# Optimization experiments

Measured on AMD Instinct MI355X. Metric: run time of the kernel, lower is better.

The kernel has to match this reference:

```python
import jax, jax.numpy as jnp
import numpy as np

L, D = 6, 2048


def setup_inputs() -> dict:
    key = jax.random.key(0)
    ks = jax.random.split(key, 6)
    # 0.05 scale keeps repeated matrix compositions numerically tame
    W_upper = jax.random.normal(ks[0], (L, D, D), dtype=jnp.float32) * 0.05
    W_lower = jax.random.normal(ks[1], (L, D, D), dtype=jnp.float32) * 0.05
    b_upper = jax.random.normal(ks[2], (L, D), dtype=jnp.float32)
    b_lower = jax.random.normal(ks[3], (L, D), dtype=jnp.float32)
    ub = jax.random.normal(ks[4], (L, D), dtype=jnp.float32)
    lb = jax.random.normal(ks[5], (L, D), dtype=jnp.float32)
    return dict(W_upper=W_upper, W_lower=W_lower, b_upper=b_upper,
                b_lower=b_lower, ub=ub, lb=lb)


def _pos(W):
    # M * W  where M = (W >= 0)
    return jnp.where(W >= 0, W, jnp.zeros_like(W))


def _neg(W):
    # ~M * W where M = (W >= 0)
    return jnp.where(W >= 0, jnp.zeros_like(W), W)


def reference(W_upper, W_lower, b_upper, b_lower, ub, lb):
    # Layer index L-1 is `self`; backsubstitute toward layer 0 (input layer).
    Wu, Wl = W_upper[-1], W_lower[-1]          # [D, D]
    bu, bl = b_upper[-1], b_lower[-1]          # [D]
    best_ub, best_lb = ub[-1], lb[-1]          # [D]
    n_layers = W_upper.shape[0]
    for i in range(n_layers - 2, -1, -1):      # prev = layer i
        Wu_p, Wu_n = _pos(Wu), _neg(Wu)
        Wl_p, Wl_n = _pos(Wl), _neg(Wl)
        # concrete bounds through prev's pre-activation bounds
        cur_ub = Wu_p @ ub[i] + Wu_n @ lb[i] + bu
        cur_lb = Wl_p @ lb[i] + Wl_n @ ub[i] + bl
        best_ub = jnp.minimum(best_ub, cur_ub)
        best_lb = jnp.maximum(best_lb, cur_lb)
        # compose symbolic bounds with prev layer's relaxation
        bu = Wu_p @ b_upper[i] + Wu_n @ b_lower[i] + bu
        bl = Wl_p @ b_lower[i] + Wl_n @ b_upper[i] + bl
        Wu = Wu_p @ W_upper[i] + Wu_n @ W_lower[i]
        Wl = Wl_p @ W_lower[i] + Wl_n @ W_upper[i]
    # final concretization against the input layer's bounds (layer 0)
    Wu_p, Wu_n = _pos(Wu), _neg(Wu)
    Wl_p, Wl_n = _pos(Wl), _neg(Wl)
    cur_ub = Wu_p @ ub[0] + Wu_n @ lb[0] + bu
    cur_lb = Wl_p @ lb[0] + Wl_n @ ub[0] + bl
    best_ub = jnp.minimum(best_ub, cur_ub)
    best_lb = jnp.maximum(best_lb, cur_lb)
    return best_ub, best_lb
```

## Files before the change

kernel.cpp:

```cpp
#include <hip/hip_runtime.h>

#define D 2048
#define DD ((size_t)D * (size_t)D)

typedef __attribute__((ext_vector_type(8))) short bf16x8;
typedef __attribute__((ext_vector_type(16))) float f32x16;

#define GLOBAL_AS __attribute__((address_space(1)))
#define LDS_AS __attribute__((address_space(3)))

__device__ inline unsigned short f2bf(float f) {
  unsigned u = __float_as_uint(f);
  u += 0x7fffu + ((u >> 16) & 1u);
  return (unsigned short)(u >> 16);
}

__global__ void init_vecs(const float* __restrict__ b_upper5,
                          const float* __restrict__ b_lower5,
                          const float* __restrict__ ub5,
                          const float* __restrict__ lb5,
                          float* __restrict__ bu, float* __restrict__ bl,
                          float* __restrict__ out) {
  int t = blockIdx.x * blockDim.x + threadIdx.x;
  if (t < D) {
    bu[t] = b_upper5[t];
    bl[t] = b_lower5[t];
    out[t] = ub5[t];
    out[D + t] = lb5[t];
  }
}

__global__ __launch_bounds__(256) void prep(
    const float* __restrict__ Wu, const float* __restrict__ Wl,
    const float* __restrict__ ubi, const float* __restrict__ lbi,
    const float* __restrict__ bupi, const float* __restrict__ bloi,
    float* __restrict__ bu, float* __restrict__ bl,
    float* __restrict__ best,
    unsigned short* __restrict__ oU, unsigned short* __restrict__ oL,
    const float* __restrict__ Wup, const float* __restrict__ Wlo,
    unsigned short* __restrict__ BsT, unsigned short* __restrict__ BdT,
    int update_bias, int write16) {
  __shared__ float red[4][4];
  __shared__ unsigned short sS[64][68];
  __shared__ unsigned short sD[64][68];

  const int t = threadIdx.x;

  if (blockIdx.x < 2048) {
    const int r = blockIdx.x;
    const size_t base = (size_t)r * D + t * 8;
    const int c = t * 8;

    float4 wu0 = *(const float4*)(Wu + base), wu1 = *(const float4*)(Wu + base + 4);
    float4 wl0 = *(const float4*)(Wl + base), wl1 = *(const float4*)(Wl + base + 4);
    float4 u0 = *(const float4*)(ubi + c),  u1 = *(const float4*)(ubi + c + 4);
    float4 l0 = *(const float4*)(lbi + c),  l1 = *(const float4*)(lbi + c + 4);
    float4 p0 = *(const float4*)(bupi + c), p1 = *(const float4*)(bupi + c + 4);
    float4 n0 = *(const float4*)(bloi + c), n1 = *(const float4*)(bloi + c + 4);

    float wu[8] = {wu0.x, wu0.y, wu0.z, wu0.w, wu1.x, wu1.y, wu1.z, wu1.w};
    float wl[8] = {wl0.x, wl0.y, wl0.z, wl0.w, wl1.x, wl1.y, wl1.z, wl1.w};
    float uu[8] = {u0.x, u0.y, u0.z, u0.w, u1.x, u1.y, u1.z, u1.w};
    float ll[8] = {l0.x, l0.y, l0.z, l0.w, l1.x, l1.y, l1.z, l1.w};
    float pp[8] = {p0.x, p0.y, p0.z, p0.w, p1.x, p1.y, p1.z, p1.w};
    float nn[8] = {n0.x, n0.y, n0.z, n0.w, n1.x, n1.y, n1.z, n1.w};

    float su_c = 0.f, su_b = 0.f, sl_c = 0.f, sl_b = 0.f;
    #pragma unroll
    for (int j = 0; j < 8; ++j) {
      su_c += wu[j] * (wu[j] >= 0.f ? uu[j] : ll[j]);
      su_b += wu[j] * (wu[j] >= 0.f ? pp[j] : nn[j]);
      sl_c += wl[j] * (wl[j] >= 0.f ? ll[j] : uu[j]);
      sl_b += wl[j] * (wl[j] >= 0.f ? nn[j] : pp[j]);
    }

    if (write16) {
      uint4 w;
      w.x = f2bf(wu[0]) | ((unsigned)f2bf(wu[1]) << 16);
      w.y = f2bf(wu[2]) | ((unsigned)f2bf(wu[3]) << 16);
      w.z = f2bf(wu[4]) | ((unsigned)f2bf(wu[5]) << 16);
      w.w = f2bf(wu[6]) | ((unsigned)f2bf(wu[7]) << 16);
      *(uint4*)(oU + base) = w;
      w.x = f2bf(wl[0]) | ((unsigned)f2bf(wl[1]) << 16);
      w.y = f2bf(wl[2]) | ((unsigned)f2bf(wl[3]) << 16);
      w.z = f2bf(wl[4]) | ((unsigned)f2bf(wl[5]) << 16);
      w.w = f2bf(wl[6]) | ((unsigned)f2bf(wl[7]) << 16);
      *(uint4*)(oL + base) = w;
    }

    #pragma unroll
    for (int off = 32; off; off >>= 1) {
      su_c += __shfl_down(su_c, off);
      su_b += __shfl_down(su_b, off);
      sl_c += __shfl_down(sl_c, off);
      sl_b += __shfl_down(sl_b, off);
    }
    int wave = t >> 6;
    if ((t & 63) == 0) {
      red[0][wave] = su_c; red[1][wave] = su_b;
      red[2][wave] = sl_c; red[3][wave] = sl_b;
    }
    __syncthreads();
    if (t == 0) {
      float a = red[0][0] + red[0][1] + red[0][2] + red[0][3];
      float b = red[1][0] + red[1][1] + red[1][2] + red[1][3];
      float cc = red[2][0] + red[2][1] + red[2][2] + red[2][3];
      float d = red[3][0] + red[3][1] + red[3][2] + red[3][3];
      float bu_old = bu[r], bl_old = bl[r];
      best[r]     = fminf(best[r],     a + bu_old);
      best[D + r] = fmaxf(best[D + r], cc + bl_old);
      if (update_bias) {
        bu[r] = b + bu_old;
        bl[r] = d + bl_old;
      }
    }
  } else {
    const int bx = blockIdx.x - 2048;
    const int k0 = (bx >> 5) * 64, c0 = (bx & 31) * 64;
    const int tx = t & 15, ty = t >> 4;
    #pragma unroll
    for (int r = 0; r < 4; ++r) {
      int kk = ty + r * 16;
      size_t g = (size_t)(k0 + kk) * D + c0 + tx * 4;
      float4 up = *(const float4*)(Wup + g);
      float4 lo = *(const float4*)(Wlo + g);
      sS[kk][tx * 4 + 0] = f2bf((up.x + lo.x) * 0.5f);
      sS[kk][tx * 4 + 1] = f2bf((up.y + lo.y) * 0.5f);
      sS[kk][tx * 4 + 2] = f2bf((up.z + lo.z) * 0.5f);
      sS[kk][tx * 4 + 3] = f2bf((up.w + lo.w) * 0.5f);
      sD[kk][tx * 4 + 0] = f2bf((up.x - lo.x) * 0.5f);
      sD[kk][tx * 4 + 1] = f2bf((up.y - lo.y) * 0.5f);
      sD[kk][tx * 4 + 2] = f2bf((up.z - lo.z) * 0.5f);
      sD[kk][tx * 4 + 3] = f2bf((up.w - lo.w) * 0.5f);
    }
    __syncthreads();
    #pragma unroll
    for (int r = 0; r < 4; ++r) {
      int cc = ty + r * 16;
      int kq = tx * 4;
      unsigned a0 = sS[kq + 0][cc] | ((unsigned)sS[kq + 1][cc] << 16);
      unsigned a1 = sS[kq + 2][cc] | ((unsigned)sS[kq + 3][cc] << 16);
      *(uint2*)(BsT + (size_t)(c0 + cc) * D + k0 + kq) = make_uint2(a0, a1);
      a0 = sD[kq + 0][cc] | ((unsigned)sD[kq + 1][cc] << 16);
      a1 = sD[kq + 2][cc] | ((unsigned)sD[kq + 3][cc] << 16);
      *(uint2*)(BdT + (size_t)(c0 + cc) * D + k0 + kq) = make_uint2(a0, a1);
    }
  }
}

__global__ __launch_bounds__(512, 2) void gemm_fused(
    const unsigned short* __restrict__ w16U,
    const unsigned short* __restrict__ w16L,
    const unsigned short* __restrict__ BsT,
    const unsigned short* __restrict__ BdT,
    float* __restrict__ Cu, float* __restrict__ Cl) {
  extern __shared__ unsigned char lds[];

  const int bid = blockIdx.x;
  const int vid = (bid & 7) * 32 + (bid >> 3);
  const int row0 = (vid >> 4) * 128, col0 = (vid & 15) * 128;

  const int tid = threadIdx.x;
  const int lane = tid & 63, wid = tid >> 6;
  const int grp = wid >> 2;
  const int w2 = wid & 3;
  const int wr = w2 >> 1, wc = w2 & 1;
  const int l31 = lane & 31, kh = lane >> 5;

  const int srow8 = lane >> 3;
  const int slot  = lane & 7;
  int rowc[2], swel[2];
  #pragma unroll
  for (int c = 0; c < 2; ++c) {
    rowc[c] = (wid + c * 8) * 8 + srow8;
    swel[c] = (slot ^ (rowc[c] & 7)) * 8;
  }
  const unsigned short* gAU[2]; const unsigned short* gAL[2];
  const unsigned short* gBs[2]; const unsigned short* gBd[2];
  #pragma unroll
  for (int c = 0; c < 2; ++c) {
    gAU[c] = w16U + (size_t)(row0 + rowc[c]) * D + swel[c];
    gAL[c] = w16L + (size_t)(row0 + rowc[c]) * D + swel[c];
    gBs[c] = BsT + (size_t)(col0 + rowc[c]) * D + swel[c];
    gBd[c] = BdT + (size_t)(col0 + rowc[c]) * D + swel[c];
  }

  f32x16 acc[2][2] = {};

  int aoff[2][4], boff[2][4];
  #pragma unroll
  for (int mb = 0; mb < 2; ++mb) {
    int ar = wr * 64 + mb * 32 + l31;
    #pragma unroll
    for (int ks = 0; ks < 4; ++ks)
      aoff[mb][ks] = ar * 128 + (((ks * 2 + kh) ^ (ar & 7)) * 16);
  }
  #pragma unroll
  for (int nb = 0; nb < 2; ++nb) {
    int bc = wc * 64 + nb * 32 + l31;
    #pragma unroll
    for (int ks = 0; ks < 4; ++ks)
      boff[nb][ks] = bc * 128 + (((ks * 2 + kh) ^ (bc & 7)) * 16);
  }

  #define STAGE(curb, kt)                                                          \
    do {                                                                           \
      unsigned bb = (unsigned)(curb) * 65536u;                                     \
      _Pragma("unroll")                                                            \
      for (int c = 0; c < 2; ++c) {                                                \
        unsigned dst = bb + (unsigned)(wid + c * 8) * 1024u;                       \
        __builtin_amdgcn_global_load_lds((const GLOBAL_AS unsigned*)(gAU[c] + (kt)),\
            (LDS_AS unsigned*)(lds + 0 + dst), 16, 0, 0);                          \
        __builtin_amdgcn_global_load_lds((const GLOBAL_AS unsigned*)(gAL[c] + (kt)),\
            (LDS_AS unsigned*)(lds + 16384 + dst), 16, 0, 0);                      \
        __builtin_amdgcn_global_load_lds((const GLOBAL_AS unsigned*)(gBs[c] + (kt)),\
            (LDS_AS unsigned*)(lds + 32768 + dst), 16, 0, 0);                      \
        __builtin_amdgcn_global_load_lds((const GLOBAL_AS unsigned*)(gBd[c] + (kt)),\
            (LDS_AS unsigned*)(lds + 49152 + dst), 16, 0, 0);                      \
      }                                                                            \
    } while (0)

  STAGE(0, 0);
  __syncthreads();

  int cur = 0;
  const unsigned Abase = grp ? 16384u : 0u;
  for (int t = 0; t < 32; ++t) {
    if (t < 31) STAGE(cur ^ 1, (t + 1) * 64);

    const unsigned char* Ab = lds + Abase + cur * 65536;
    const unsigned char* Sb = lds + 32768 + cur * 65536;
    const unsigned char* Db = lds + 49152 + cur * 65536;

    #pragma unroll
    for (int ks = 0; ks < 4; ++ks) {
      bf16x8 aw0 = *(const bf16x8*)(Ab + aoff[0][ks]);
      bf16x8 aw1 = *(const bf16x8*)(Ab + aoff[1][ks]);
      bf16x8 bs0 = *(const bf16x8*)(Sb + boff[0][ks]);
      bf16x8 bs1 = *(const bf16x8*)(Sb + boff[1][ks]);
      bf16x8 bd0 = *(const bf16x8*)(Db + boff[0][ks]);
      bf16x8 bd1 = *(const bf16x8*)(Db + boff[1][ks]);
      if (grp) { bd0 ^= (short)0x8000; bd1 ^= (short)0x8000; }
      bf16x8 av0 = aw0 & (short)0x7fff;
      bf16x8 av1 = aw1 & (short)0x7fff;

      acc[0][0] = __builtin_amdgcn_mfma_f32_32x32x16_bf16(aw0, bs0, acc[0][0], 0, 0, 0);
      acc[0][0] = __builtin_amdgcn_mfma_f32_32x32x16_bf16(av0, bd0, acc[0][0], 0, 0, 0);
      acc[0][1] = __builtin_amdgcn_mfma_f32_32x32x16_bf16(aw0, bs1, acc[0][1], 0, 0, 0);
      acc[0][1] = __builtin_amdgcn_mfma_f32_32x32x16_bf16(av0, bd1, acc[0][1], 0, 0, 0);
      acc[1][0] = __builtin_amdgcn_mfma_f32_32x32x16_bf16(aw1, bs0, acc[1][0], 0, 0, 0);
      acc[1][0] = __builtin_amdgcn_mfma_f32_32x32x16_bf16(av1, bd0, acc[1][0], 0, 0, 0);
      acc[1][1] = __builtin_amdgcn_mfma_f32_32x32x16_bf16(aw1, bs1, acc[1][1], 0, 0, 0);
      acc[1][1] = __builtin_amdgcn_mfma_f32_32x32x16_bf16(av1, bd1, acc[1][1], 0, 0, 0);
    }

    __syncthreads();
    cur ^= 1;
  }
  #undef STAGE

  float* C = grp ? Cl : Cu;
  #pragma unroll
  for (int mb = 0; mb < 2; ++mb)
    #pragma unroll
    for (int nb = 0; nb < 2; ++nb) {
      const int colg = col0 + wc * 64 + nb * 32 + l31;
      const int rowb = row0 + wr * 64 + mb * 32 + kh * 4;
      #pragma unroll
      for (int g = 0; g < 4; ++g)
        #pragma unroll
        for (int j = 0; j < 4; ++j)
          C[(size_t)(rowb + g * 8 + j) * D + colg] = acc[mb][nb][g * 4 + j];
    }
}

extern "C" void kernel_launch(void* const* d_in, const int* in_sizes, int n_in,
                              void* d_out, int out_size, void* d_ws, size_t ws_size,
                              hipStream_t stream) {
  const float* W_upper = (const float*)d_in[0];
  const float* W_lower = (const float*)d_in[1];
  const float* b_upper = (const float*)d_in[2];
  const float* b_lower = (const float*)d_in[3];
  const float* ub      = (const float*)d_in[4];
  const float* lb      = (const float*)d_in[5];
  float* out = (float*)d_out;
  float* ws  = (float*)d_ws;

  float* curU = ws;
  float* curL = ws + DD;
  unsigned short* w16U = (unsigned short*)(ws + 2 * DD);
  unsigned short* w16L = w16U + DD;
  unsigned short* BsT  = w16L + DD;
  unsigned short* BdT  = BsT + DD;
  float* bu = (float*)(BdT + DD);
  float* bl = bu + D;

  static_cast<void>(hipFuncSetAttribute(
      (const void*)gemm_fused, hipFuncAttributeMaxDynamicSharedMemorySize, 131072));

  init_vecs<<<(D + 255) / 256, 256, 0, stream>>>(
      b_upper + 5 * D, b_lower + 5 * D, ub + 5 * D, lb + 5 * D, bu, bl, out);

  const float* cU = W_upper + 5 * DD;
  const float* cL = W_lower + 5 * DD;
  for (int i = 4; i >= 0; --i) {
    prep<<<3072, 256, 0, stream>>>(cU, cL, ub + (size_t)i * D, lb + (size_t)i * D,
                                   b_upper + (size_t)i * D, b_lower + (size_t)i * D,
                                   bu, bl, out, w16U, w16L,
                                   W_upper + (size_t)i * DD, W_lower + (size_t)i * DD,
                                   BsT, BdT, 1, 1);
    gemm_fused<<<256, 512, 131072, stream>>>(w16U, w16L, BsT, BdT, curU, curL);
    cU = curU; cL = curL;
  }
  prep<<<2048, 256, 0, stream>>>(cU, cL, ub, lb, b_upper, b_lower,
                                 bu, bl, out, w16U, w16L,
                                 (const float*)nullptr, (const float*)nullptr,
                                 (unsigned short*)nullptr, (unsigned short*)nullptr,
                                 0, 0);
}
```

Measured before the change: 460.1 us.

## Use four-stage LDS pipeline with smaller K tiles and interleaved async loads

Result: slower. 510.6 us (+11.0%).

```diff
diff --git a/kernel.cpp b/kernel.cpp
--- a/kernel.cpp
+++ b/kernel.cpp
@@ -167,83 +167,83 @@
   const int wr = w2 >> 1, wc = w2 & 1;
   const int l31 = lane & 31, kh = lane >> 5;
 
-  const int srow8 = lane >> 3;
-  const int slot  = lane & 7;
-  int rowc[2], swel[2];
-  #pragma unroll
-  for (int c = 0; c < 2; ++c) {
-    rowc[c] = (wid + c * 8) * 8 + srow8;
-    swel[c] = (slot ^ (rowc[c] & 7)) * 8;
-  }
-  const unsigned short* gAU[2]; const unsigned short* gAL[2];
-  const unsigned short* gBs[2]; const unsigned short* gBd[2];
-  #pragma unroll
-  for (int c = 0; c < 2; ++c) {
-    gAU[c] = w16U + (size_t)(row0 + rowc[c]) * D + swel[c];
-    gAL[c] = w16L + (size_t)(row0 + rowc[c]) * D + swel[c];
-    gBs[c] = BsT + (size_t)(col0 + rowc[c]) * D + swel[c];
-    gBd[c] = BdT + (size_t)(col0 + rowc[c]) * D + swel[c];
-  }
+  const int rowc = wid * 16 + (lane >> 2);
+  const int swel = ((lane & 3) ^ (rowc & 3)) * 8;
+  const unsigned short* gAU = w16U + (size_t)(row0 + rowc) * D + swel;
+  const unsigned short* gAL = w16L + (size_t)(row0 + rowc) * D + swel;
+  const unsigned short* gBs = BsT + (size_t)(col0 + rowc) * D + swel;
+  const unsigned short* gBd = BdT + (size_t)(col0 + rowc) * D + swel;
 
   f32x16 acc[2][2] = {};
 
-  int aoff[2][4], boff[2][4];
+  int aoff[2][2], boff[2][2];
   #pragma unroll
   for (int mb = 0; mb < 2; ++mb) {
     int ar = wr * 64 + mb * 32 + l31;
     #pragma unroll
-    for (int ks = 0; ks < 4; ++ks)
-      aoff[mb][ks] = ar * 128 + (((ks * 2 + kh) ^ (ar & 7)) * 16);
+    for (int ks = 0; ks < 2; ++ks)
+      aoff[mb][ks] = ar * 64 + (((ks * 2 + kh) ^ (ar & 3)) * 16);
   }
   #pragma unroll
   for (int nb = 0; nb < 2; ++nb) {
     int bc = wc * 64 + nb * 32 + l31;
     #pragma unroll
-    for (int ks = 0; ks < 4; ++ks)
-      boff[nb][ks] = bc * 128 + (((ks * 2 + kh) ^ (bc & 7)) * 16);
-  }
-
-  #define STAGE(curb, kt)                                                          \
-    do {                                                                           \
-      unsigned bb = (unsigned)(curb) * 65536u;                                     \
-      _Pragma("unroll")                                                            \
-      for (int c = 0; c < 2; ++c) {                                                \
-        unsigned dst = bb + (unsigned)(wid + c * 8) * 1024u;                       \
-        __builtin_amdgcn_global_load_lds((const GLOBAL_AS unsigned*)(gAU[c] + (kt)),\
-            (LDS_AS unsigned*)(lds + 0 + dst), 16, 0, 0);                          \
-        __builtin_amdgcn_global_load_lds((const GLOBAL_AS unsigned*)(gAL[c] + (kt)),\
-            (LDS_AS unsigned*)(lds + 16384 + dst), 16, 0, 0);                      \
-        __builtin_amdgcn_global_load_lds((const GLOBAL_AS unsigned*)(gBs[c] + (kt)),\
-            (LDS_AS unsigned*)(lds + 32768 + dst), 16, 0, 0);                      \
-        __builtin_amdgcn_global_load_lds((const GLOBAL_AS unsigned*)(gBd[c] + (kt)),\
-            (LDS_AS unsigned*)(lds + 49152 + dst), 16, 0, 0);                      \
-      }                                                                            \
+    for (int ks = 0; ks < 2; ++ks)
+      boff[nb][ks] = bc * 64 + (((ks * 2 + kh) ^ (bc & 3)) * 16);
+  }
+
+  #define STAGE_A(buf, kt)                                                        \
+    do {                                                                          \
+      unsigned dst = (unsigned)(buf) * 32768u + (unsigned)wid * 1024u;            \
+      __builtin_amdgcn_global_load_lds((const GLOBAL_AS unsigned*)(gAU + (kt)),   \
+          (LDS_AS unsigned*)(lds + 0 + dst), 16, 0, 0);                           \
+      __builtin_amdgcn_global_load_lds((const GLOBAL_AS unsigned*)(gAL + (kt)),   \
+          (LDS_AS unsigned*)(lds + 8192 + dst), 16, 0, 0);                        \
     } while (0)
-
-  STAGE(0, 0);
-  __syncthreads();
-
-  int cur = 0;
-  const unsigned Abase = grp ? 16384u : 0u;
-  for (int t = 0; t < 32; ++t) {
-    if (t < 31) STAGE(cur ^ 1, (t + 1) * 64);
-
-    const unsigned char* Ab = lds + Abase + cur * 65536;
-    const unsigned char* Sb = lds + 32768 + cur * 65536;
-    const unsigned char* Db = lds + 49152 + cur * 65536;
-
-    #pragma unroll
-    for (int ks = 0; ks < 4; ++ks) {
+  #define STAGE_B(buf, kt)                                                        \
+    do {                                                                          \
+      unsigned dst = (unsigned)(buf) * 32768u + (unsigned)wid * 1024u;            \
+      __builtin_amdgcn_global_load_lds((const GLOBAL_AS unsigned*)(gBs + (kt)),   \
+          (LDS_AS unsigned*)(lds + 16384 + dst), 16, 0, 0);                       \
+      __builtin_amdgcn_global_load_lds((const GLOBAL_AS unsigned*)(gBd + (kt)),   \
+          (LDS_AS unsigned*)(lds + 24576 + dst), 16, 0, 0);                       \
+    } while (0)
+
+  STAGE_A(0, 0);  STAGE_B(0, 0);
+  STAGE_A(1, 32); STAGE_B(1, 32);
+  STAGE_A(2, 64); STAGE_B(2, 64);
+
+  const unsigned Abase = grp ? 8192u : 0u;
+  for (int t = 0; t < 64; ++t) {
+    if (t < 62)       asm volatile("s_waitcnt vmcnt(8)" ::: "memory");
+    else if (t == 62) asm volatile("s_waitcnt vmcnt(4)" ::: "memory");
+    else              asm volatile("s_waitcnt vmcnt(0)" ::: "memory");
+    __builtin_amdgcn_s_barrier();
+
+    const unsigned char* Ab = lds + Abase + (t & 3) * 32768;
+    const unsigned char* Sb = lds + 16384 + (t & 3) * 32768;
+    const unsigned char* Db = lds + 24576 + (t & 3) * 32768;
+    const bool do_stage = (t <= 60);
+
+    #pragma unroll
+    for (int ks = 0; ks < 2; ++ks) {
       bf16x8 aw0 = *(const bf16x8*)(Ab + aoff[0][ks]);
       bf16x8 aw1 = *(const bf16x8*)(Ab + aoff[1][ks]);
       bf16x8 bs0 = *(const bf16x8*)(Sb + boff[0][ks]);
       bf16x8 bs1 = *(const bf16x8*)(Sb + boff[1][ks]);
       bf16x8 bd0 = *(const bf16x8*)(Db + boff[0][ks]);
       bf16x8 bd1 = *(const bf16x8*)(Db + boff[1][ks]);
+
+      if (do_stage) {
+        if (ks == 0) STAGE_A((t + 3) & 3, (t + 3) * 32);
+        else         STAGE_B((t + 3) & 3, (t + 3) * 32);
+      }
+
       if (grp) { bd0 ^= (short)0x8000; bd1 ^= (short)0x8000; }
       bf16x8 av0 = aw0 & (short)0x7fff;
       bf16x8 av1 = aw1 & (short)0x7fff;
 
+      __builtin_amdgcn_s_setprio(1);
       acc[0][0] = __builtin_amdgcn_mfma_f32_32x32x16_bf16(aw0, bs0, acc[0][0], 0, 0, 0);
       acc[0][0] = __builtin_amdgcn_mfma_f32_32x32x16_bf16(av0, bd0, acc[0][0], 0, 0, 0);
       acc[0][1] = __builtin_amdgcn_mfma_f32_32x32x16_bf16(aw0, bs1, acc[0][1], 0, 0, 0);
@@ -252,12 +252,11 @@
       acc[1][0] = __builtin_amdgcn_mfma_f32_32x32x16_bf16(av1, bd0, acc[1][0], 0, 0, 0);
       acc[1][1] = __builtin_amdgcn_mfma_f32_32x32x16_bf16(aw1, bs1, acc[1][1], 0, 0, 0);
       acc[1][1] = __builtin_amdgcn_mfma_f32_32x32x16_bf16(av1, bd1, acc[1][1], 0, 0, 0);
-    }
-
-    __syncthreads();
-    cur ^= 1;
-  }
-  #undef STAGE
+      __builtin_amdgcn_s_setprio(0);
+    }
+  }
+  #undef STAGE_A
+  #undef STAGE_B
 
   float* C = grp ? Cl : Cu;
   #pragma unroll
```

## Split tile prefetch into halves with fine-grained waitcnt and barrier scheduling

Applied to the files above, without the earlier changes.

Measured after the change: 490.5 us. 1.07x slower.

```diff
diff --git a/kernel.cpp b/kernel.cpp
--- a/kernel.cpp
+++ b/kernel.cpp
@@ -167,23 +167,13 @@
   const int wr = w2 >> 1, wc = w2 & 1;
   const int l31 = lane & 31, kh = lane >> 5;
 
-  const int srow8 = lane >> 3;
-  const int slot  = lane & 7;
-  int rowc[2], swel[2];
-  #pragma unroll
-  for (int c = 0; c < 2; ++c) {
-    rowc[c] = (wid + c * 8) * 8 + srow8;
-    swel[c] = (slot ^ (rowc[c] & 7)) * 8;
-  }
-  const unsigned short* gAU[2]; const unsigned short* gAL[2];
-  const unsigned short* gBs[2]; const unsigned short* gBd[2];
-  #pragma unroll
-  for (int c = 0; c < 2; ++c) {
-    gAU[c] = w16U + (size_t)(row0 + rowc[c]) * D + swel[c];
-    gAL[c] = w16L + (size_t)(row0 + rowc[c]) * D + swel[c];
-    gBs[c] = BsT + (size_t)(col0 + rowc[c]) * D + swel[c];
-    gBd[c] = BdT + (size_t)(col0 + rowc[c]) * D + swel[c];
-  }
+  const int rowh = wid * 8 + (lane >> 3);
+  const int slot = lane & 7;
+  const int swel = (slot ^ (rowh & 7)) * 8;
+  const unsigned short* gAU = w16U + (size_t)(row0 + rowh) * D + swel;
+  const unsigned short* gAL = w16L + (size_t)(row0 + rowh) * D + swel;
+  const unsigned short* gBs = BsT + (size_t)(col0 + rowh) * D + swel;
+  const unsigned short* gBd = BdT + (size_t)(col0 + rowh) * D + swel;
 
   f32x16 acc[2][2] = {};
 
@@ -203,47 +193,59 @@
       boff[nb][ks] = bc * 128 + (((ks * 2 + kh) ^ (bc & 7)) * 16);
   }
 
-  #define STAGE(curb, kt)                                                          \
+  #define STAGE_HALF(bu_, h, kt)                                                   \
     do {                                                                           \
-      unsigned bb = (unsigned)(curb) * 65536u;                                     \
-      _Pragma("unroll")                                                            \
-      for (int c = 0; c < 2; ++c) {                                                \
-        unsigned dst = bb + (unsigned)(wid + c * 8) * 1024u;                       \
-        __builtin_amdgcn_global_load_lds((const GLOBAL_AS unsigned*)(gAU[c] + (kt)),\
-            (LDS_AS unsigned*)(lds + 0 + dst), 16, 0, 0);                          \
-        __builtin_amdgcn_global_load_lds((const GLOBAL_AS unsigned*)(gAL[c] + (kt)),\
-            (LDS_AS unsigned*)(lds + 16384 + dst), 16, 0, 0);                      \
-        __builtin_amdgcn_global_load_lds((const GLOBAL_AS unsigned*)(gBs[c] + (kt)),\
-            (LDS_AS unsigned*)(lds + 32768 + dst), 16, 0, 0);                      \
-        __builtin_amdgcn_global_load_lds((const GLOBAL_AS unsigned*)(gBd[c] + (kt)),\
-            (LDS_AS unsigned*)(lds + 49152 + dst), 16, 0, 0);                      \
-      }                                                                            \
+      unsigned dst = (unsigned)(bu_) * 65536u + (unsigned)(h) * 8192u +            \
+                     (unsigned)wid * 1024u;                                        \
+      size_t so = (size_t)(h) * 64 * D + (size_t)(kt);                             \
+      __builtin_amdgcn_global_load_lds((const GLOBAL_AS unsigned*)(gAU + so),      \
+          (LDS_AS unsigned*)(lds + 0 + dst), 16, 0, 0);                            \
+      __builtin_amdgcn_global_load_lds((const GLOBAL_AS unsigned*)(gAL + so),      \
+          (LDS_AS unsigned*)(lds + 16384 + dst), 16, 0, 0);                        \
+      __builtin_amdgcn_global_load_lds((const GLOBAL_AS unsigned*)(gBs + so),      \
+          (LDS_AS unsigned*)(lds + 32768 + dst), 16, 0, 0);                        \
+      __builtin_amdgcn_global_load_lds((const GLOBAL_AS unsigned*)(gBd + so),      \
+          (LDS_AS unsigned*)(lds + 49152 + dst), 16, 0, 0);                        \
     } while (0)
 
-  STAGE(0, 0);
-  __syncthreads();
-
-  int cur = 0;
+  STAGE_HALF(0, 0, 0);
+  STAGE_HALF(0, 1, 0);
+
   const unsigned Abase = grp ? 16384u : 0u;
   for (int t = 0; t < 32; ++t) {
-    if (t < 31) STAGE(cur ^ 1, (t + 1) * 64);
-
-    const unsigned char* Ab = lds + Abase + cur * 65536;
-    const unsigned char* Sb = lds + 32768 + cur * 65536;
-    const unsigned char* Db = lds + 49152 + cur * 65536;
-
-    #pragma unroll
-    for (int ks = 0; ks < 4; ++ks) {
-      bf16x8 aw0 = *(const bf16x8*)(Ab + aoff[0][ks]);
-      bf16x8 aw1 = *(const bf16x8*)(Ab + aoff[1][ks]);
-      bf16x8 bs0 = *(const bf16x8*)(Sb + boff[0][ks]);
-      bf16x8 bs1 = *(const bf16x8*)(Sb + boff[1][ks]);
-      bf16x8 bd0 = *(const bf16x8*)(Db + boff[0][ks]);
-      bf16x8 bd1 = *(const bf16x8*)(Db + boff[1][ks]);
+    const int buf = t & 1;
+    if (t < 31) {
+      STAGE_HALF(buf ^ 1, 0, (t + 1) * 64);
+      asm volatile("s_waitcnt vmcnt(4)" ::: "memory");
+    } else {
+      asm volatile("s_waitcnt vmcnt(0)" ::: "memory");
+    }
+    __builtin_amdgcn_s_barrier();
+
+    const unsigned char* Ab = lds + Abase + (unsigned)buf * 65536u;
+    const unsigned char* Sb = lds + 32768u + (unsigned)buf * 65536u;
+    const unsigned char* Db = lds + 49152u + (unsigned)buf * 65536u;
+
+    #pragma unroll
+    for (int p = 0; p < 4; ++p) {
+      bf16x8 aw0 = *(const bf16x8*)(Ab + aoff[0][p]);
+      bf16x8 aw1 = *(const bf16x8*)(Ab + aoff[1][p]);
+      bf16x8 bs0 = *(const bf16x8*)(Sb + boff[0][p]);
+      bf16x8 bs1 = *(const bf16x8*)(Sb + boff[1][p]);
+      bf16x8 bd0 = *(const bf16x8*)(Db + boff[0][p]);
+      bf16x8 bd1 = *(const bf16x8*)(Db + boff[1][p]);
+
+      if (p == 2 && t < 31) STAGE_HALF(buf ^ 1, 1, (t + 1) * 64);
+
+      __builtin_amdgcn_s_barrier();
+      asm volatile("s_waitcnt lgkmcnt(0)" ::: "memory");
+      __builtin_amdgcn_sched_barrier(0);
+
       if (grp) { bd0 ^= (short)0x8000; bd1 ^= (short)0x8000; }
       bf16x8 av0 = aw0 & (short)0x7fff;
       bf16x8 av1 = aw1 & (short)0x7fff;
 
+      __builtin_amdgcn_s_setprio(1);
       acc[0][0] = __builtin_amdgcn_mfma_f32_32x32x16_bf16(aw0, bs0, acc[0][0], 0, 0, 0);
       acc[0][0] = __builtin_amdgcn_mfma_f32_32x32x16_bf16(av0, bd0, acc[0][0], 0, 0, 0);
       acc[0][1] = __builtin_amdgcn_mfma_f32_32x32x16_bf16(aw0, bs1, acc[0][1], 0, 0, 0);
@@ -252,12 +254,11 @@
       acc[1][0] = __builtin_amdgcn_mfma_f32_32x32x16_bf16(av1, bd0, acc[1][0], 0, 0, 0);
       acc[1][1] = __builtin_amdgcn_mfma_f32_32x32x16_bf16(aw1, bs1, acc[1][1], 0, 0, 0);
       acc[1][1] = __builtin_amdgcn_mfma_f32_32x32x16_bf16(av1, bd1, acc[1][1], 0, 0, 0);
-    }
-
-    __syncthreads();
-    cur ^= 1;
-  }
-  #undef STAGE
+      __builtin_amdgcn_s_setprio(0);
+      __builtin_amdgcn_s_barrier();
+    }
+  }
+  #undef STAGE_HALF
 
   float* C = grp ? Cl : Cu;
   #pragma unroll
```

## Split fused upper/lower GEMM into separate half-blocks with smaller K tile

Applied to the files above, without the earlier changes.

Result: slower. 526.3 us (+14.4%).

```diff
diff --git a/kernel.cpp b/kernel.cpp
--- a/kernel.cpp
+++ b/kernel.cpp
@@ -148,7 +148,7 @@
   }
 }
 
-__global__ __launch_bounds__(512, 2) void gemm_fused(
+__global__ __launch_bounds__(256, 2) void gemm_half(
     const unsigned short* __restrict__ w16U,
     const unsigned short* __restrict__ w16L,
     const unsigned short* __restrict__ BsT,
@@ -157,83 +157,78 @@
   extern __shared__ unsigned char lds[];
 
   const int bid = blockIdx.x;
-  const int vid = (bid & 7) * 32 + (bid >> 3);
-  const int row0 = (vid >> 4) * 128, col0 = (vid & 15) * 128;
+  const int x = bid & 7, j = bid >> 3;
+  const int grp = j & 1;
+  const int tile = x * 32 + (j >> 1);
+  const int row0 = (tile >> 4) * 128, col0 = (tile & 15) * 128;
 
   const int tid = threadIdx.x;
   const int lane = tid & 63, wid = tid >> 6;
-  const int grp = wid >> 2;
-  const int w2 = wid & 3;
-  const int wr = w2 >> 1, wc = w2 & 1;
+  const int wr = wid >> 1, wc = wid & 1;
   const int l31 = lane & 31, kh = lane >> 5;
 
-  const int srow8 = lane >> 3;
-  const int slot  = lane & 7;
+  const unsigned short* Aown = grp ? w16L : w16U;
+
   int rowc[2], swel[2];
   #pragma unroll
   for (int c = 0; c < 2; ++c) {
-    rowc[c] = (wid + c * 8) * 8 + srow8;
-    swel[c] = (slot ^ (rowc[c] & 7)) * 8;
-  }
-  const unsigned short* gAU[2]; const unsigned short* gAL[2];
-  const unsigned short* gBs[2]; const unsigned short* gBd[2];
+    rowc[c] = (wid + c * 4) * 16 + (lane >> 2);
+    swel[c] = ((lane & 3) ^ ((rowc[c] >> 1) & 3)) * 8;
+  }
+  const unsigned short* gA[2]; const unsigned short* gBs[2];
+  const unsigned short* gBd[2];
   #pragma unroll
   for (int c = 0; c < 2; ++c) {
-    gAU[c] = w16U + (size_t)(row0 + rowc[c]) * D + swel[c];
-    gAL[c] = w16L + (size_t)(row0 + rowc[c]) * D + swel[c];
+    gA[c]  = Aown + (size_t)(row0 + rowc[c]) * D + swel[c];
     gBs[c] = BsT + (size_t)(col0 + rowc[c]) * D + swel[c];
     gBd[c] = BdT + (size_t)(col0 + rowc[c]) * D + swel[c];
   }
 
   f32x16 acc[2][2] = {};
 
-  int aoff[2][4], boff[2][4];
+  int aoff[2][2], boff[2][2];
   #pragma unroll
   for (int mb = 0; mb < 2; ++mb) {
     int ar = wr * 64 + mb * 32 + l31;
     #pragma unroll
-    for (int ks = 0; ks < 4; ++ks)
-      aoff[mb][ks] = ar * 128 + (((ks * 2 + kh) ^ (ar & 7)) * 16);
+    for (int ks = 0; ks < 2; ++ks)
+      aoff[mb][ks] = ar * 64 + (((ks * 2 + kh) ^ ((ar >> 1) & 3)) * 16);
   }
   #pragma unroll
   for (int nb = 0; nb < 2; ++nb) {
     int bc = wc * 64 + nb * 32 + l31;
     #pragma unroll
-    for (int ks = 0; ks < 4; ++ks)
-      boff[nb][ks] = bc * 128 + (((ks * 2 + kh) ^ (bc & 7)) * 16);
-  }
-
-  #define STAGE(curb, kt)                                                          \
-    do {                                                                           \
-      unsigned bb = (unsigned)(curb) * 65536u;                                     \
-      _Pragma("unroll")                                                            \
-      for (int c = 0; c < 2; ++c) {                                                \
-        unsigned dst = bb + (unsigned)(wid + c * 8) * 1024u;                       \
-        __builtin_amdgcn_global_load_lds((const GLOBAL_AS unsigned*)(gAU[c] + (kt)),\
-            (LDS_AS unsigned*)(lds + 0 + dst), 16, 0, 0);                          \
-        __builtin_amdgcn_global_load_lds((const GLOBAL_AS unsigned*)(gAL[c] + (kt)),\
-            (LDS_AS unsigned*)(lds + 16384 + dst), 16, 0, 0);                      \
+    for (int ks = 0; ks < 2; ++ks)
+      boff[nb][ks] = bc * 64 + (((ks * 2 + kh) ^ ((bc >> 1) & 3)) * 16);
+  }
+
+  #define STAGE(buf, kt)                                                          \
+    do {                                                                          \
+      _Pragma("unroll")                                                           \
+      for (int c = 0; c < 2; ++c) {                                               \
+        unsigned dst = (unsigned)(buf) * 24576u + (unsigned)(wid + c * 4) * 1024u;\
+        __builtin_amdgcn_global_load_lds((const GLOBAL_AS unsigned*)(gA[c] + (kt)),\
+            (LDS_AS unsigned*)(lds + 0 + dst), 16, 0, 0);                         \
         __builtin_amdgcn_global_load_lds((const GLOBAL_AS unsigned*)(gBs[c] + (kt)),\
-            (LDS_AS unsigned*)(lds + 32768 + dst), 16, 0, 0);                      \
+            (LDS_AS unsigned*)(lds + 8192 + dst), 16, 0, 0);                      \
         __builtin_amdgcn_global_load_lds((const GLOBAL_AS unsigned*)(gBd[c] + (kt)),\
-            (LDS_AS unsigned*)(lds + 49152 + dst), 16, 0, 0);                      \
-      }                                                                            \
+            (LDS_AS unsigned*)(lds + 16384 + dst), 16, 0, 0);                     \
+      }                                                                           \
     } while (0)
 
   STAGE(0, 0);
   __syncthreads();
 
-  int cur = 0;
-  const unsigned Abase = grp ? 16384u : 0u;
-  for (int t = 0; t < 32; ++t) {
-    if (t < 31) STAGE(cur ^ 1, (t + 1) * 64);
-
-    const unsigned char* Ab = lds + Abase + cur * 65536;
-    const unsigned char* Sb = lds + 32768 + cur * 65536;
-    const unsigned char* Db = lds + 49152 + cur * 65536;
-
-    #pragma unroll
-    for (int ks = 0; ks < 4; ++ks) {
+  int buf = 0;
+  for (int t = 0; t < 64; ++t) {
+    if (t < 63) STAGE(buf ^ 1, (t + 1) * 32);
+
+    const unsigned char* Ab = lds + (unsigned)buf * 24576u;
+    const unsigned char* Sb = Ab + 8192;
+    const unsigned char* Db = Ab + 16384;
+
+    #pragma unroll
+    for (int ks = 0; ks < 2; ++ks) {
       bf16x8 aw0 = *(const bf16x8*)(Ab + aoff[0][ks]);
       bf16x8 aw1 = *(const bf16x8*)(Ab + aoff[1][ks]);
       bf16x8 bs0 = *(const bf16x8*)(Sb + boff[0][ks]);
@@ -255,7 +250,7 @@
     }
 
     __syncthreads();
-    cur ^= 1;
+    buf ^= 1;
   }
   #undef STAGE
 
@@ -269,8 +264,8 @@
       #pragma unroll
       for (int g = 0; g < 4; ++g)
         #pragma unroll
-        for (int j = 0; j < 4; ++j)
-          C[(size_t)(rowb + g * 8 + j) * D + colg] = acc[mb][nb][g * 4 + j];
+        for (int j2 = 0; j2 < 4; ++j2)
+          C[(size_t)(rowb + g * 8 + j2) * D + colg] = acc[mb][nb][g * 4 + j2];
     }
 }
 
@@ -296,7 +291,7 @@
   float* bl = bu + D;
 
   static_cast<void>(hipFuncSetAttribute(
-      (const void*)gemm_fused, hipFuncAttributeMaxDynamicSharedMemorySize, 131072));
+      (const void*)gemm_half, hipFuncAttributeMaxDynamicSharedMemorySize, 49152));
 
   init_vecs<<<(D + 255) / 256, 256, 0, stream>>>(
       b_upper + 5 * D, b_lower + 5 * D, ub + 5 * D, lb + 5 * D, bu, bl, out);
@@ -309,7 +304,7 @@
                                    bu, bl, out, w16U, w16L,
                                    W_upper + (size_t)i * DD, W_lower + (size_t)i * DD,
                                    BsT, BdT, 1, 1);
-    gemm_fused<<<256, 512, 131072, stream>>>(w16U, w16L, BsT, BdT, curU, curL);
+    gemm_half<<<512, 256, 49152, stream>>>(w16U, w16L, BsT, BdT, curU, curL);
     cU = curU; cL = curL;
   }
   prep<<<2048, 256, 0, stream>>>(cU, cL, ub, lb, b_upper, b_lower,
```
